# Performance work log

Measured on AMD Instinct MI355X. Metric: run time of the kernel, lower is better.

## Reference

```python
import jax, jax.numpy as jnp
import numpy as np

DIM = 256
HEADS = 4
HEAD_DIM = 32
HIDDEN = HEADS * HEAD_DIM  # 128
EPS = 1e-12  # F.normalize eps


def rmsnorm(x, g):
    # F.normalize(x, dim=1) * g * sqrt(C)
    n = jnp.sqrt(jnp.sum(x * x, axis=1, keepdims=True))
    return x / jnp.maximum(n, EPS) * g * jnp.sqrt(jnp.float32(x.shape[1]))


def setup_inputs() -> dict:
    key = jax.random.key(0)
    k1, k2, k3 = jax.random.split(key, 3)
    b, h, w = 16, 64, 64
    x = jax.random.normal(k1, (b, DIM, h, w), dtype=jnp.float32)
    # conv weights: kaiming-ish scale for 1x1 convs
    w_qkv = jax.random.normal(k2, (3 * HIDDEN, DIM), dtype=jnp.float32) / np.sqrt(DIM)
    w_out = jax.random.normal(k3, (DIM, HIDDEN), dtype=jnp.float32) / np.sqrt(HIDDEN)
    return {
        "x": x,
        "g_norm": jnp.ones((1, DIM, 1, 1), jnp.float32),
        "w_qkv": w_qkv,
        "w_out": w_out,
        "b_out": jnp.zeros((DIM,), jnp.float32),
        "g_out": jnp.ones((1, DIM, 1, 1), jnp.float32),
    }


def reference(x, g_norm, w_qkv, w_out, b_out, g_out):
    b, c, h, w = x.shape
    n = h * w
    scale = HEAD_DIM ** (-0.5)

    xn = rmsnorm(x, g_norm)
    # 1x1 conv == channel matmul: (3*hidden, c) x (b, c, h, w)
    qkv = jnp.einsum('oc,bchw->bohw', w_qkv, xn)
    qkv = qkv.reshape(b, 3, HEADS, HEAD_DIM, n)
    q, k, v = qkv[:, 0], qkv[:, 1], qkv[:, 2]  # each (b, heads, head_dim, n)

    q = jax.nn.softmax(q, axis=-2)  # over head_dim
    k = jax.nn.softmax(k, axis=-1)  # over spatial tokens

    # context = k @ v^T : (b, heads, d, d)
    context = jnp.einsum('bhdn,bhen->bhde', k, v)
    # out = context^T @ (q*scale) : (b, heads, d, n)
    out = jnp.einsum('bhde,bhdn->bhen', context, q * scale)
    out = out.reshape(b, HIDDEN, h, w)

    out = jnp.einsum('oc,bchw->bohw', w_out, out) + b_out[None, :, None, None]
    out = rmsnorm(out, g_out)
    return out
```

## Files before the change

### kernel.cpp

```cpp
#include <hip/hip_runtime.h>
#include <hip/hip_bf16.h>
#include <math.h>

#define B 16
#define C 256
#define H 4
#define D 32
#define HID 128
#define O3 384
#define N 4096
#define NSPLIT 32
#define QSCALE 0.17677669529663687f
#define RMS_MUL 16.0f
#define EPS 1e-12f

typedef __attribute__((ext_vector_type(8))) short short8;
typedef __attribute__((ext_vector_type(4))) float f32x4;

#define VM0_BARRIER() asm volatile("s_waitcnt vmcnt(0)\ns_barrier" ::: "memory")

__device__ __forceinline__ ushort f2bf(float f) {
  __hip_bfloat16 h = __float2bfloat16(f);
  return *(ushort*)&h;
}
__device__ __forceinline__ void load_lds16(const void* g, void* l) {
  __builtin_amdgcn_global_load_lds((const __attribute__((address_space(1))) void*)g,
                                   (__attribute__((address_space(3))) void*)l, 16, 0, 0);
}

__global__ __launch_bounds__(256) void k_prep(const float* __restrict__ wqkv,
                                              const float* __restrict__ g,
                                              const float* __restrict__ x,
                                              ushort* __restrict__ wA,
                                              ushort* __restrict__ xbf) {
  __shared__ float red[8][32];
  __shared__ float invs[32];
  int t = threadIdx.x;
  if (blockIdx.x < 384) {
    int idx = blockIdx.x * 256 + t;
    wA[idx] = f2bf(wqkv[idx] * g[idx & (C - 1)]);
    return;
  }
  int id = blockIdx.x - 384;
  int g8 = t >> 5, ln = t & 31;
  int b = id >> 7, n0 = (id & 127) * 32;
  const float* xb = x + (size_t)b * C * N + n0 + ln;
  float v[32];
  float ss = 0.f;
  #pragma unroll
  for (int i = 0; i < 32; ++i) {
    v[i] = xb[(size_t)(g8 * 32 + i) * N];
    ss += v[i] * v[i];
  }
  red[g8][ln] = ss;
  __syncthreads();
  if (t < 32) {
    float tot = 0.f;
    #pragma unroll
    for (int j = 0; j < 8; ++j) tot += red[j][t];
    invs[t] = RMS_MUL / fmaxf(sqrtf(tot), EPS);
  }
  __syncthreads();
  float inv = invs[ln];
  ushort* dst = xbf + ((size_t)(b * N + n0 + ln)) * C + g8 * 32;
  #pragma unroll
  for (int ch = 0; ch < 4; ++ch) {
    union { ushort s[8]; uint4 q; } u;
    #pragma unroll
    for (int j = 0; j < 8; ++j) u.s[j] = f2bf(v[ch * 8 + j] * inv);
    *(uint4*)(dst + ch * 8) = u.q;
  }
}

__global__ __launch_bounds__(256, 4) void k_kvctx(const ushort* __restrict__ A,
                                                  const ushort* __restrict__ Bm,
                                                  float* __restrict__ ctxp) {
  const int K = 256;
  __shared__ ushort lds[16384];
  int bid = blockIdx.x;
  int work = (bid & 7) * 128 + (bid >> 3);
  int mh = work & 1, sl = (work >> 1) & 31, b = work >> 6;
  int t = threadIdx.x;
  int lane = t & 63, w = t >> 6;
  int n0 = sl * 128;
  const ushort* Bb = Bm + ((size_t)b * N + n0) * K;
  f32x4 acc[2][8] = {};

  auto stage = [&](int buf, int k0) {
    #pragma unroll
    for (int i = 0; i < 2; ++i) {
      int c = w * 2 + i;
      int lr = c * 16 + (lane >> 2);
      int gr = mh * 64 + (lr & 63) + ((lr & 64) << 1);
      int col = k0 + (lane & 3) * 8;
      load_lds16(A + (size_t)gr * K + col, lds + buf * 4096 + c * 512);
    }
    #pragma unroll
    for (int i = 0; i < 2; ++i) {
      int c = w * 2 + i;
      int row = c * 16 + (lane >> 2);
      int col = k0 + (lane & 3) * 8;
      load_lds16(Bb + (size_t)row * K + col, lds + 8192 + buf * 4096 + c * 512);
    }
  };

  stage(0, 0);
  VM0_BARRIER();
  #pragma unroll
  for (int ki = 0; ki < 8; ++ki) {
    int cur = ki & 1;
    if (ki < 7) stage(cur ^ 1, (ki + 1) * 32);
    const ushort* Ar = lds + cur * 4096;
    const ushort* Br = lds + 8192 + cur * 4096;
    short8 af[2], bfr[8];
    #pragma unroll
    for (int m = 0; m < 2; ++m)
      af[m] = *(const short8*)&Ar[(w * 32 + m * 16 + (lane & 15)) * 32 + (lane >> 4) * 8];
    #pragma unroll
    for (int nn = 0; nn < 8; ++nn)
      bfr[nn] = *(const short8*)&Br[(nn * 16 + (lane & 15)) * 32 + (lane >> 4) * 8];
    #pragma unroll
    for (int m = 0; m < 2; ++m)
      #pragma unroll
      for (int nn = 0; nn < 8; ++nn)
        acc[m][nn] = __builtin_amdgcn_mfma_f32_16x16x32_bf16(af[m], bfr[nn], acc[m][nn], 0, 0, 0);
    VM0_BARRIER();
  }

  float* cbb = ctxp + (size_t)(sl * 64 + b * 4) * 1056;
  if (w < 2) {
    #pragma unroll
    for (int m = 0; m < 2; ++m)
      #pragma unroll
      for (int nn = 0; nn < 8; ++nn)
        #pragma unroll
        for (int j = 0; j < 4; ++j) acc[m][nn][j] = __expf(acc[m][nn][j]);
    #pragma unroll
    for (int m = 0; m < 2; ++m)
      #pragma unroll
      for (int j = 0; j < 4; ++j) {
        float s = 0.f;
        #pragma unroll
        for (int nn = 0; nn < 8; ++nn) s += acc[m][nn][j];
        s += __shfl_xor(s, 1); s += __shfl_xor(s, 2);
        s += __shfl_xor(s, 4); s += __shfl_xor(s, 8);
        if ((lane & 15) == 0) {
          int lr = w * 32 + m * 16 + (lane >> 4) * 4 + j;
          int h = mh * 2 + (lr >> 5);
          cbb[(size_t)h * 1056 + 1024 + (lr & 31)] = s;
        }
      }
  }
  #pragma unroll
  for (int m = 0; m < 2; ++m)
    #pragma unroll
    for (int nn = 0; nn < 8; ++nn) {
      int lr0 = w * 32 + m * 16 + (lane >> 4) * 4;
      int n = nn * 16 + (lane & 15);
      #pragma unroll
      for (int j = 0; j < 4; ++j) {
        int lr = lr0 + j;
        lds[(lr * 128 + n) ^ ((lr & 7) << 3)] = f2bf(acc[m][nn][j]);
      }
    }
  __syncthreads();
  int hl = w >> 1, eh = w & 1;
  f32x4 cacc[2] = {};
  #pragma unroll
  for (int kk = 0; kk < 4; ++kk) {
    short8 af2[2], bv;
    #pragma unroll
    for (int m = 0; m < 2; ++m) {
      int lrk = hl * 32 + m * 16 + (lane & 15);
      af2[m] = *(const short8*)&lds[(lrk * 128 + kk * 32 + (lane >> 4) * 8) ^ ((lrk & 7) << 3)];
    }
    int lrv = 64 + hl * 32 + eh * 16 + (lane & 15);
    bv = *(const short8*)&lds[(lrv * 128 + kk * 32 + (lane >> 4) * 8) ^ ((lrv & 7) << 3)];
    #pragma unroll
    for (int m = 0; m < 2; ++m)
      cacc[m] = __builtin_amdgcn_mfma_f32_16x16x32_bf16(af2[m], bv, cacc[m], 0, 0, 0);
  }
  int hg = mh * 2 + hl;
  float* cb = ctxp + (size_t)(sl * 64 + b * 4 + hg) * 1056;
  #pragma unroll
  for (int m = 0; m < 2; ++m)
    #pragma unroll
    for (int j = 0; j < 4; ++j) {
      int d = m * 16 + (lane >> 4) * 4 + j;
      int e = eh * 16 + (lane & 15);
      cb[d * 32 + e] = cacc[m][j];
    }
}

__global__ __launch_bounds__(256) void k_redweff(const float* __restrict__ ctxp,
                                                 const float* __restrict__ wout,
                                                 ushort* __restrict__ Weff) {
  __shared__ float ctxn[D][D + 1];
  __shared__ float ksum[D];
  int bh = blockIdx.x;
  int b = bh >> 2, h = bh & 3;
  int t = threadIdx.x;
  int d = t >> 3, e0 = (t & 7) * 4;
  float vs[4] = {0.f, 0.f, 0.f, 0.f};
  float ks = 0.f;
  for (int s = 0; s < NSPLIT; ++s) {
    const float* cb = ctxp + (size_t)(s * 64 + bh) * 1056;
    f32x4 v = *(const f32x4*)(cb + d * 32 + e0);
    vs[0] += v[0]; vs[1] += v[1]; vs[2] += v[2]; vs[3] += v[3];
    if (t < 32) ks += cb[1024 + t];
  }
  if (t < 32) ksum[t] = ks;
  __syncthreads();
  float rk = 1.f / ksum[d];
  #pragma unroll
  for (int j = 0; j < 4; ++j) ctxn[d][e0 + j] = vs[j] * rk;
  __syncthreads();
  float wrow[D];
  #pragma unroll
  for (int e = 0; e < D; ++e) wrow[e] = wout[t * HID + h * D + e];
  ushort* wb = Weff + ((size_t)(b * C + t)) * HID + h * D;
  #pragma unroll
  for (int g = 0; g < 4; ++g) {
    union { ushort s[8]; uint4 v; } u;
    #pragma unroll
    for (int dj = 0; dj < 8; ++dj) {
      int dd = g * 8 + dj;
      float a = 0.f;
      #pragma unroll
      for (int e = 0; e < D; ++e) a += wrow[e] * ctxn[dd][e];
      u.s[dj] = f2bf(a);
    }
    *(uint4*)(wb + g * 8) = u.v;
  }
}

__global__ __launch_bounds__(256, 4) void k_qout(const ushort* __restrict__ A,
                                                 const ushort* __restrict__ Bm,
                                                 const ushort* __restrict__ WeffG,
                                                 const float* __restrict__ bias,
                                                 const float* __restrict__ g,
                                                 float* __restrict__ outp) {
  const int K = 256;
  __shared__ ushort lds[16384];
  ushort* qlds = lds + 8192;
  int bid = blockIdx.x;
  int work = (bid & 7) * 128 + (bid >> 3);
  int xt = work & 63, b = work >> 6;
  int t = threadIdx.x;
  int lane = t & 63, w = t >> 6;
  int n0 = xt * 64;
  const ushort* Bb = Bm + ((size_t)b * N + n0) * K;
  {
    auto stage1 = [&](int buf, int k0) {
      #pragma unroll
      for (int i = 0; i < 2; ++i) {
        int c = w * 2 + i;
        int row = c * 16 + (lane >> 2);
        int col = k0 + (lane & 3) * 8;
        load_lds16(A + (size_t)row * K + col, lds + buf * 4096 + c * 512);
      }
      {
        int c = w;
        int row = c * 16 + (lane >> 2);
        int col = k0 + (lane & 3) * 8;
        load_lds16(Bb + (size_t)row * K + col, lds + 8192 + buf * 2048 + c * 512);
      }
    };
    f32x4 acc[2][4] = {};
    stage1(0, 0);
    VM0_BARRIER();
    #pragma unroll
    for (int ki = 0; ki < 8; ++ki) {
      int cur = ki & 1;
      if (ki < 7) stage1(cur ^ 1, (ki + 1) * 32);
      const ushort* Ar = lds + cur * 4096;
      const ushort* Br = lds + 8192 + cur * 2048;
      short8 af[2], bfr[4];
      #pragma unroll
      for (int m = 0; m < 2; ++m)
        af[m] = *(const short8*)&Ar[(w * 32 + m * 16 + (lane & 15)) * 32 + (lane >> 4) * 8];
      #pragma unroll
      for (int nn = 0; nn < 4; ++nn)
        bfr[nn] = *(const short8*)&Br[(nn * 16 + (lane & 15)) * 32 + (lane >> 4) * 8];
      #pragma unroll
      for (int m = 0; m < 2; ++m)
        #pragma unroll
        for (int nn = 0; nn < 4; ++nn)
          acc[m][nn] = __builtin_amdgcn_mfma_f32_16x16x32_bf16(af[m], bfr[nn], acc[m][nn], 0, 0, 0);
      VM0_BARRIER();
    }
    #pragma unroll
    for (int nn = 0; nn < 4; ++nn) {
      float pm = -1e30f;
      #pragma unroll
      for (int m = 0; m < 2; ++m)
        #pragma unroll
        for (int j = 0; j < 4; ++j) pm = fmaxf(pm, acc[m][nn][j]);
      pm = fmaxf(pm, __shfl_xor(pm, 16));
      pm = fmaxf(pm, __shfl_xor(pm, 32));
      float e[2][4], ps = 0.f;
      #pragma unroll
      for (int m = 0; m < 2; ++m)
        #pragma unroll
        for (int j = 0; j < 4; ++j) {
          e[m][j] = __expf(acc[m][nn][j] - pm);
          ps += e[m][j];
        }
      ps += __shfl_xor(ps, 16);
      ps += __shfl_xor(ps, 32);
      float rs = QSCALE / ps;
      #pragma unroll
      for (int m = 0; m < 2; ++m)
        #pragma unroll
        for (int j = 0; j < 4; ++j) acc[m][nn][j] = e[m][j] * rs;
    }
    #pragma unroll
    for (int m = 0; m < 2; ++m)
      #pragma unroll
      for (int nn = 0; nn < 4; ++nn) {
        int d0 = w * 32 + m * 16 + (lane >> 4) * 4;
        int n = nn * 16 + (lane & 15);
        union { ushort us[4]; uint2 v; } u;
        #pragma unroll
        for (int j = 0; j < 4; ++j) u.us[j] = f2bf(acc[m][nn][j]);
        *(uint2*)&qlds[(n * 128 + d0) ^ ((n & 7) << 3)] = u.v;
      }
  }
  __syncthreads();
  const ushort* Aw = WeffG + (size_t)b * C * HID;
  ushort* A2buf = lds;
  f32x4 acc2[4][4] = {};
  for (int k0 = 0; k0 < HID; k0 += 32) {
    #pragma unroll
    for (int i = 0; i < 4; ++i) {
      int c = w * 4 + i;
      int row = c * 16 + (lane >> 2);
      int col = k0 + (lane & 3) * 8;
      load_lds16(Aw + (size_t)row * HID + col, A2buf + c * 512);
    }
    __syncthreads();
    short8 af[4], bfr[4];
    #pragma unroll
    for (int m = 0; m < 4; ++m)
      af[m] = *(const short8*)&A2buf[(w * 64 + m * 16 + (lane & 15)) * 32 + (lane >> 4) * 8];
    #pragma unroll
    for (int nn = 0; nn < 4; ++nn) {
      int n = nn * 16 + (lane & 15);
      bfr[nn] = *(const short8*)&qlds[(n * 128 + k0 + (lane >> 4) * 8) ^ ((n & 7) << 3)];
    }
    #pragma unroll
    for (int m = 0; m < 4; ++m)
      #pragma unroll
      for (int nn = 0; nn < 4; ++nn)
        acc2[m][nn] = __builtin_amdgcn_mfma_f32_16x16x32_bf16(af[m], bfr[nn], acc2[m][nn], 0, 0, 0);
    __syncthreads();
  }
  float* ssred = (float*)lds;
  #pragma unroll
  for (int m = 0; m < 4; ++m)
    #pragma unroll
    for (int j = 0; j < 4; ++j) {
      int row = w * 64 + m * 16 + (lane >> 4) * 4 + j;
      float bv = bias[row];
      #pragma unroll
      for (int nn = 0; nn < 4; ++nn) acc2[m][nn][j] += bv;
    }
  float ssp[4];
  #pragma unroll
  for (int nn = 0; nn < 4; ++nn) {
    float s = 0.f;
    #pragma unroll
    for (int m = 0; m < 4; ++m)
      #pragma unroll
      for (int j = 0; j < 4; ++j) s += acc2[m][nn][j] * acc2[m][nn][j];
    s += __shfl_xor(s, 16);
    s += __shfl_xor(s, 32);
    ssp[nn] = s;
  }
  if ((lane >> 4) == 0) {
    #pragma unroll
    for (int nn = 0; nn < 4; ++nn) ssred[w * 64 + nn * 16 + (lane & 15)] = ssp[nn];
  }
  __syncthreads();
  float inv[4];
  #pragma unroll
  for (int nn = 0; nn < 4; ++nn) {
    int col = nn * 16 + (lane & 15);
    float tot = ssred[col] + ssred[64 + col] + ssred[128 + col] + ssred[192 + col];
    inv[nn] = RMS_MUL / fmaxf(sqrtf(tot), EPS);
  }
  float* Cb = outp + (size_t)b * C * N + n0;
  #pragma unroll
  for (int m = 0; m < 4; ++m)
    #pragma unroll
    for (int j = 0; j < 4; ++j) {
      int row = w * 64 + m * 16 + (lane >> 4) * 4 + j;
      float gm = g[row];
      #pragma unroll
      for (int nn = 0; nn < 4; ++nn) {
        int col = nn * 16 + (lane & 15);
        Cb[(size_t)row * N + col] = acc2[m][nn][j] * inv[nn] * gm;
      }
    }
}

extern "C" void kernel_launch(void* const* d_in, const int* in_sizes, int n_in,
                              void* d_out, int out_size, void* d_ws, size_t ws_size,
                              hipStream_t stream) {
  const float* x    = (const float*)d_in[0];
  const float* gn   = (const float*)d_in[1];
  const float* wqkv = (const float*)d_in[2];
  const float* wout = (const float*)d_in[3];
  const float* bout = (const float*)d_in[4];
  const float* gout = (const float*)d_in[5];
  float* out = (float*)d_out;
  float* ws  = (float*)d_ws;

  ushort* xbf  = (ushort*)ws;
  float*  ctxp = ws + 8388608;
  ushort* Weff = (ushort*)(ws + 10551296);
  ushort* wA   = (ushort*)(ws + 10813440);

  k_prep   <<<2432, 256, 0, stream>>>(wqkv, gn, x, wA, xbf);
  k_kvctx  <<<1024, 256, 0, stream>>>(wA + 128 * 256, xbf, ctxp);
  k_redweff<<<64, 256, 0, stream>>>(ctxp, wout, Weff);
  k_qout   <<<1024, 256, 0, stream>>>(wA, xbf, Weff, bout, gout, out);
}
```

Before: 85.09 us.

## Fuse context reduction into kvctx via last-block atomic counter; prefetch Weff tiles

Removes the separate k_redweff launch. Each kvctx block now bumps an atomic counter per (batch, head-pair), and the last of the 32 split blocks reduces the partial contexts and builds Weff. Counters are zeroed in k_prep. In k_qout, the first Weff tile is staged before the softmax epilogue and later tiles are issued after each MFMA step, which overlaps those loads with compute. This saves a launch and some idle gaps, but the final reduction is serialized inside the last-arriving block.

After: 204.0 us. +139.8%, slower.

```diff
diff --git a/kernel.cpp b/kernel.cpp
--- a/kernel.cpp
+++ b/kernel.cpp
@@ -32,11 +32,13 @@
                                               const float* __restrict__ g,
                                               const float* __restrict__ x,
                                               ushort* __restrict__ wA,
-                                              ushort* __restrict__ xbf) {
+                                              ushort* __restrict__ xbf,
+                                              int* __restrict__ counters) {
   __shared__ float red[8][32];
   __shared__ float invs[32];
   int t = threadIdx.x;
   if (blockIdx.x < 384) {
+    if (blockIdx.x == 0 && t < 32) counters[t] = 0;
     int idx = blockIdx.x * 256 + t;
     wA[idx] = f2bf(wqkv[idx] * g[idx & (C - 1)]);
     return;
@@ -74,9 +76,13 @@
 
 __global__ __launch_bounds__(256, 4) void k_kvctx(const ushort* __restrict__ A,
                                                   const ushort* __restrict__ Bm,
-                                                  float* __restrict__ ctxp) {
+                                                  const float* __restrict__ wout,
+                                                  float* __restrict__ ctxp,
+                                                  ushort* __restrict__ Weff,
+                                                  int* __restrict__ counters) {
   const int K = 256;
   __shared__ ushort lds[16384];
+  __shared__ int lastflag;
   int bid = blockIdx.x;
   int work = (bid & 7) * 128 + (bid >> 3);
   int mh = work & 1, sl = (work >> 1) & 31, b = work >> 6;
@@ -190,47 +196,52 @@
       int e = eh * 16 + (lane & 15);
       cb[d * 32 + e] = cacc[m][j];
     }
-}
-
-__global__ __launch_bounds__(256) void k_redweff(const float* __restrict__ ctxp,
-                                                 const float* __restrict__ wout,
-                                                 ushort* __restrict__ Weff) {
-  __shared__ float ctxn[D][D + 1];
-  __shared__ float ksum[D];
-  int bh = blockIdx.x;
-  int b = bh >> 2, h = bh & 3;
-  int t = threadIdx.x;
-  int d = t >> 3, e0 = (t & 7) * 4;
-  float vs[4] = {0.f, 0.f, 0.f, 0.f};
-  float ks = 0.f;
-  for (int s = 0; s < NSPLIT; ++s) {
-    const float* cb = ctxp + (size_t)(s * 64 + bh) * 1056;
-    f32x4 v = *(const f32x4*)(cb + d * 32 + e0);
-    vs[0] += v[0]; vs[1] += v[1]; vs[2] += v[2]; vs[3] += v[3];
-    if (t < 32) ks += cb[1024 + t];
-  }
-  if (t < 32) ksum[t] = ks;
-  __syncthreads();
-  float rk = 1.f / ksum[d];
-  #pragma unroll
-  for (int j = 0; j < 4; ++j) ctxn[d][e0 + j] = vs[j] * rk;
-  __syncthreads();
-  float wrow[D];
-  #pragma unroll
-  for (int e = 0; e < D; ++e) wrow[e] = wout[t * HID + h * D + e];
-  ushort* wb = Weff + ((size_t)(b * C + t)) * HID + h * D;
-  #pragma unroll
-  for (int g = 0; g < 4; ++g) {
-    union { ushort s[8]; uint4 v; } u;
-    #pragma unroll
-    for (int dj = 0; dj < 8; ++dj) {
-      int dd = g * 8 + dj;
-      float a = 0.f;
-      #pragma unroll
-      for (int e = 0; e < D; ++e) a += wrow[e] * ctxn[dd][e];
-      u.s[dj] = f2bf(a);
-    }
-    *(uint4*)(wb + g * 8) = u.v;
+
+  __threadfence();
+  if (t == 0)
+    lastflag = (atomicAdd(&counters[b * 2 + mh], 1) == 31);
+  __syncthreads();
+  if (lastflag) {
+    __threadfence();
+    float* ctxn = (float*)lds;
+    float* ksum = (float*)lds + 1056;
+    int d = t >> 3, e0 = (t & 7) * 4;
+    for (int hh = 0; hh < 2; ++hh) {
+      int h = mh * 2 + hh;
+      int bh = b * 4 + h;
+      __syncthreads();
+      float vs[4] = {0.f, 0.f, 0.f, 0.f};
+      float ks = 0.f;
+      for (int s = 0; s < NSPLIT; ++s) {
+        const float* cp = ctxp + (size_t)(s * 64 + bh) * 1056;
+        f32x4 v = *(const f32x4*)(cp + d * 32 + e0);
+        vs[0] += v[0]; vs[1] += v[1]; vs[2] += v[2]; vs[3] += v[3];
+        if (t < 32) ks += cp[1024 + t];
+      }
+      if (t < 32) ksum[t] = ks;
+      __syncthreads();
+      float rk = 1.f / ksum[d];
+      #pragma unroll
+      for (int j = 0; j < 4; ++j) ctxn[d * 33 + e0 + j] = vs[j] * rk;
+      __syncthreads();
+      float wrow[D];
+      #pragma unroll
+      for (int e = 0; e < D; ++e) wrow[e] = wout[t * HID + h * D + e];
+      ushort* wb = Weff + ((size_t)(b * C + t)) * HID + h * D;
+      #pragma unroll
+      for (int gq = 0; gq < 4; ++gq) {
+        union { ushort s[8]; uint4 v; } u;
+        #pragma unroll
+        for (int dj = 0; dj < 8; ++dj) {
+          int dd = gq * 8 + dj;
+          float a = 0.f;
+          #pragma unroll
+          for (int e = 0; e < D; ++e) a += wrow[e] * ctxn[dd * 33 + e];
+          u.s[dj] = f2bf(a);
+        }
+        *(uint4*)(wb + gq * 8) = u.v;
+      }
+    }
   }
 }
 
@@ -250,6 +261,19 @@
   int lane = t & 63, w = t >> 6;
   int n0 = xt * 64;
   const ushort* Bb = Bm + ((size_t)b * N + n0) * K;
+  const ushort* Aw = WeffG + (size_t)b * C * HID;
+  ushort* A2buf = lds;
+
+  auto stage2 = [&](int k0) {
+    #pragma unroll
+    for (int i = 0; i < 4; ++i) {
+      int c = w * 4 + i;
+      int row = c * 16 + (lane >> 2);
+      int col = k0 + (lane & 3) * 8;
+      load_lds16(Aw + (size_t)row * HID + col, A2buf + c * 512);
+    }
+  };
+
   {
     auto stage1 = [&](int buf, int k0) {
       #pragma unroll
@@ -289,6 +313,7 @@
           acc[m][nn] = __builtin_amdgcn_mfma_f32_16x16x32_bf16(af[m], bfr[nn], acc[m][nn], 0, 0, 0);
       VM0_BARRIER();
     }
+    stage2(0);
     #pragma unroll
     for (int nn = 0; nn < 4; ++nn) {
       float pm = -1e30f;
@@ -327,18 +352,8 @@
       }
   }
   __syncthreads();
-  const ushort* Aw = WeffG + (size_t)b * C * HID;
-  ushort* A2buf = lds;
   f32x4 acc2[4][4] = {};
   for (int k0 = 0; k0 < HID; k0 += 32) {
-    #pragma unroll
-    for (int i = 0; i < 4; ++i) {
-      int c = w * 4 + i;
-      int row = c * 16 + (lane >> 2);
-      int col = k0 + (lane & 3) * 8;
-      load_lds16(Aw + (size_t)row * HID + col, A2buf + c * 512);
-    }
-    __syncthreads();
     short8 af[4], bfr[4];
     #pragma unroll
     for (int m = 0; m < 4; ++m)
@@ -353,8 +368,13 @@
       #pragma unroll
       for (int nn = 0; nn < 4; ++nn)
         acc2[m][nn] = __builtin_amdgcn_mfma_f32_16x16x32_bf16(af[m], bfr[nn], acc2[m][nn], 0, 0, 0);
-    __syncthreads();
-  }
+    if (k0 < HID - 32) {
+      __syncthreads();
+      stage2(k0 + 32);
+      VM0_BARRIER();
+    }
+  }
+  __syncthreads();
   float* ssred = (float*)lds;
   #pragma unroll
   for (int m = 0; m < 4; ++m)
@@ -416,13 +436,13 @@
   float* out = (float*)d_out;
   float* ws  = (float*)d_ws;
 
-  ushort* xbf  = (ushort*)ws;
-  float*  ctxp = ws + 8388608;
-  ushort* Weff = (ushort*)(ws + 10551296);
-  ushort* wA   = (ushort*)(ws + 10813440);
-
-  k_prep   <<<2432, 256, 0, stream>>>(wqkv, gn, x, wA, xbf);
-  k_kvctx  <<<1024, 256, 0, stream>>>(wA + 128 * 256, xbf, ctxp);
-  k_redweff<<<64, 256, 0, stream>>>(ctxp, wout, Weff);
-  k_qout   <<<1024, 256, 0, stream>>>(wA, xbf, Weff, bout, gout, out);
-}
+  ushort* xbf     = (ushort*)ws;
+  float*  ctxp    = ws + 8388608;
+  ushort* Weff    = (ushort*)(ws + 10551296);
+  ushort* wA      = (ushort*)(ws + 10813440);
+  int*    counters = (int*)(ws + 10862592);
+
+  k_prep <<<2432, 256, 0, stream>>>(wqkv, gn, x, wA, xbf, counters);
+  k_kvctx<<<1024, 256, 0, stream>>>(wA + 128 * 256, xbf, wout, ctxp, Weff, counters);
+  k_qout <<<1024, 256, 0, stream>>>(wA, xbf, Weff, bout, gout, out);
+}
```
